# Kernel optimization log

Measured on AMD Instinct MI355X. Metric: run time of the kernel, lower is better.

Reference implementation:

```python
import jax, jax.numpy as jnp
import numpy as np

# dims: batch B, seq T, d_model C, expert_hidden H, n_experts E (top-1 routing)
B, T, C, H, E = 1, 256, 1024, 2048, 8
STD = 0.02


def setup_inputs() -> dict:
    key = jax.random.key(0)
    ks = jax.random.split(key, 8)
    f32 = jnp.float32
    return {
        "x": jax.random.normal(ks[0], (B, T, C), f32),
        "up": jax.random.normal(ks[1], (E, H, C), f32) * STD,
        "gate": jax.random.normal(ks[2], (E, H, C), f32) * STD,
        "down": jax.random.normal(ks[3], (E, C, H), f32) * STD,
        "router": jax.random.normal(ks[4], (E, C), f32) * STD,
        "w_up_s": jax.random.normal(ks[5], (H, C), f32) * STD,
        "w_gate_s": jax.random.normal(ks[6], (H, C), f32) * STD,
        "w_down_s": jax.random.normal(ks[7], (C, H), f32) * STD,
    }


def reference(x, up, gate, down, router, w_up_s, w_gate_s, w_down_s):
    b, t, c = x.shape
    x_ = x.reshape(b * t, c)                      # [BT, C]
    # top-1 router (gates are implicitly 1.0)
    logits = x_ @ router.T                        # [BT, E]
    idx = jnp.argmax(logits, axis=-1)             # [BT]
    onehot = jax.nn.one_hot(idx, router.shape[0], dtype=x.dtype)  # [BT, E]
    # dense all-expert SwiGLU, combined with one-hot (same math as per-token gather)
    u = jnp.einsum('bc,ehc->ebh', x_, up)         # [E, BT, H]
    g = jnp.einsum('bc,ehc->ebh', x_, gate)       # [E, BT, H]
    h = jax.nn.silu(g) * u                        # [E, BT, H]
    ye = jnp.einsum('ebh,ech->ebc', h, down)      # [E, BT, C]
    y = jnp.einsum('ebc,be->bc', ye, onehot)      # [BT, C]
    # shared expert residual
    ys = (jax.nn.silu(x_ @ w_gate_s.T) * (x_ @ w_up_s.T)) @ w_down_s.T
    return (y + ys).reshape(b, t, c)
```

## Files before the change

### kernel.cpp

```cpp
#include <hip/hip_runtime.h>
#include <hip/hip_bf16.h>

#define T_TOK 256
#define C_DIM 1024
#define H_DIM 2048
#define E_NUM 8

typedef __attribute__((ext_vector_type(4))) float f32x4;
typedef __attribute__((ext_vector_type(8))) short short8;

#define WS_CNT    0
#define WS_LIST   1024
#define WS_XBF    16384
#define WS_HBUF   (1u<<20)
#define WS_HSBUF  (2u<<20)
#define WS_YS     (3u<<20)

__device__ __forceinline__ ushort f2bf(float f) {
    __hip_bfloat16 h = __float2bfloat16(f);
    return *reinterpret_cast<ushort*>(&h);
}

__device__ __forceinline__ ushort4 f2bf4(float4 v) {
    ushort4 r; r.x = f2bf(v.x); r.y = f2bf(v.y); r.z = f2bf(v.z); r.w = f2bf(v.w);
    return r;
}

__device__ __forceinline__ ushort4 f2bf4v(f32x4 v) {
    ushort4 r; r.x = f2bf(v[0]); r.y = f2bf(v[1]); r.z = f2bf(v[2]); r.w = f2bf(v[3]);
    return r;
}

__device__ __forceinline__ void gload16(const void* g, void* l) {
    __builtin_amdgcn_global_load_lds((const __attribute__((address_space(1))) void*)g,
                                     (__attribute__((address_space(3))) void*)l, 16, 0, 0);
}

#define MFMA(a, b, c) __builtin_amdgcn_mfma_f32_16x16x32_bf16((a), (b), (c), 0, 0, 0)

#define VMWAIT(N) do { asm volatile("s_waitcnt vmcnt(" #N ")" ::: "memory"); \
                       __builtin_amdgcn_sched_barrier(0); } while (0)
#define LGKWAIT() do { asm volatile("s_waitcnt lgkmcnt(0)" ::: "memory"); \
                       __builtin_amdgcn_sched_barrier(0); } while (0)
#define BAR() do { __builtin_amdgcn_s_barrier(); \
                   __builtin_amdgcn_sched_barrier(0); } while (0)

__global__ __launch_bounds__(256) void router_kernel(
    const float* __restrict__ x, const float* __restrict__ router,
    int* __restrict__ cnt, int* __restrict__ list, ushort* __restrict__ xbf)
{
    const int t = blockIdx.x;
    const int tid = threadIdx.x;
    float4 xv = reinterpret_cast<const float4*>(x + (size_t)t * C_DIM)[tid];
    *reinterpret_cast<ushort4*>(xbf + (size_t)t * C_DIM + tid * 4) = f2bf4(xv);

    float p[E_NUM];
#pragma unroll
    for (int e = 0; e < E_NUM; e++) {
        float4 rv = reinterpret_cast<const float4*>(router + (size_t)e * C_DIM)[tid];
        p[e] = xv.x * rv.x + xv.y * rv.y + xv.z * rv.z + xv.w * rv.w;
    }
#pragma unroll
    for (int e = 0; e < E_NUM; e++) {
#pragma unroll
        for (int off = 32; off >= 1; off >>= 1)
            p[e] += __shfl_down(p[e], off, 64);
    }
    __shared__ float red[E_NUM][4];
    const int lane = tid & 63, wv = tid >> 6;
    if (lane == 0) {
#pragma unroll
        for (int e = 0; e < E_NUM; e++) red[e][wv] = p[e];
    }
    __syncthreads();
    if (tid == 0) {
        float best = -3.4e38f; int bi = 0;
#pragma unroll
        for (int e = 0; e < E_NUM; e++) {
            float v = red[e][0] + red[e][1] + red[e][2] + red[e][3];
            if (v > best) { best = v; bi = e; }
        }
        int pos = atomicAdd(&cnt[bi], 1);
        list[bi * T_TOK + pos] = t;
    }
}

__global__ __launch_bounds__(256, 3) void ug_mfma(
    const ushort* __restrict__ xbf, const float* __restrict__ up, const float* __restrict__ gate,
    const float* __restrict__ w_up_s, const float* __restrict__ w_gate_s,
    const int* __restrict__ cnt, const int* __restrict__ list,
    ushort* __restrict__ hbuf, ushort* __restrict__ hsbuf)
{
    const int e = blockIdx.x, by = blockIdx.y, tt = blockIdx.z;
    const bool sh = (e == E_NUM);
    const int n = sh ? T_TOK : cnt[e];
    if (tt * 32 >= n) return;
    const int tid = threadIdx.x, lane = tid & 63, wv = tid >> 6;
    const int lc = lane & 15, kg = lane >> 4;

    __shared__ __align__(16) char smem[32768];
    ushort* Xl  = (ushort*)smem;
    ushort* WuL = (ushort*)(smem + 16384);
    ushort* WgL = (ushort*)(smem + 24576);
    __shared__ int toks_s[32];

    if (tid < 32) {
        int t = tt * 32 + tid;
        toks_s[tid] = (t < n) ? (sh ? t : list[e * T_TOK + t]) : -1;
    }
    __syncthreads();

    const int h0 = by * 16;
    const float* __restrict__ ubase = (sh ? w_up_s   : up   + (size_t)e * H_DIM * C_DIM) + (size_t)h0 * C_DIM;
    const float* __restrict__ gbase = (sh ? w_gate_s : gate + (size_t)e * H_DIM * C_DIM) + (size_t)h0 * C_DIM;

    f32x4 wreg[8];
#define W_LOAD(tc) do { _Pragma("unroll") for (int i = 0; i < 8; i++) { \
        int row_ = wv * 4 + (i & 3); \
        const float* b_ = (i < 4) ? ubase : gbase; \
        const f32x4* p_ = reinterpret_cast<const f32x4*>(b_ + (size_t)row_ * C_DIM + (tc) * 256 + lane * 4); \
        wreg[i] = (sh || i < 4) ? *p_ : __builtin_nontemporal_load(p_); \
    } } while (0)

#define W_WRITE() do { _Pragma("unroll") for (int i = 0; i < 8; i++) { \
        int row_ = wv * 4 + (i & 3); \
        ushort* WL_ = (i < 4) ? WuL : WgL; \
        int pos_ = ((lane >> 1) & ~7) | (((lane >> 1) ^ row_) & 7); \
        *reinterpret_cast<ushort4*>(WL_ + row_ * 256 + pos_ * 8 + (lane & 1) * 4) = f2bf4v(wreg[i]); \
    } } while (0)

#define X_STAGE(tc) do { _Pragma("unroll") for (int i = 0; i < 4; i++) { \
        int j_ = wv * 4 + i; \
        int row_ = 2 * j_ + (lane >> 5); \
        int p_ = lane & 31; \
        int su_ = (p_ & ~7) | ((p_ ^ row_) & 7); \
        int tok_ = toks_s[row_]; if (tok_ < 0) tok_ = 0; \
        gload16(xbf + (size_t)tok_ * C_DIM + (tc) * 256 + su_ * 8, (void*)(Xl + j_ * 512)); \
    } } while (0)

    f32x4 au0 = {0,0,0,0}, au1 = {0,0,0,0}, ag0 = {0,0,0,0}, ag1 = {0,0,0,0};
#define COMPUTE() do { _Pragma("unroll") for (int k32 = 0; k32 < 2; k32++) { \
        int ku_ = wv * 8 + k32 * 4 + kg; \
        int up_ = (ku_ & ~7) | ((ku_ ^ lc) & 7); \
        short8 a0_ = *reinterpret_cast<const short8*>(Xl + lc * 256 + up_ * 8); \
        short8 a1_ = *reinterpret_cast<const short8*>(Xl + (16 + lc) * 256 + up_ * 8); \
        short8 bu_ = *reinterpret_cast<const short8*>(WuL + lc * 256 + up_ * 8); \
        short8 bg_ = *reinterpret_cast<const short8*>(WgL + lc * 256 + up_ * 8); \
        au0 = MFMA(a0_, bu_, au0); au1 = MFMA(a1_, bu_, au1); \
        ag0 = MFMA(a0_, bg_, ag0); ag1 = MFMA(a1_, bg_, ag1); \
    } } while (0)

    W_LOAD(0);
#pragma unroll
    for (int t = 0; t < 4; t++) {
        X_STAGE(t);
        W_WRITE();
        if (t < 3) W_LOAD(t + 1);
        __syncthreads();
        COMPUTE();
        __syncthreads();
    }
#undef W_LOAD
#undef W_WRITE
#undef X_STAGE
#undef COMPUTE

    f32x4* red = (f32x4*)smem;
    red[(wv * 4 + 0) * 64 + lane] = au0;
    red[(wv * 4 + 1) * 64 + lane] = au1;
    red[(wv * 4 + 2) * 64 + lane] = ag0;
    red[(wv * 4 + 3) * 64 + lane] = ag1;
    __syncthreads();
    if (tid < 128) {
        const int m = tid >> 6, ln = tid & 63, lc_ = ln & 15, kg_ = ln >> 4;
        f32x4 su = red[(0 + m) * 64 + ln];
        su += red[(4 + m) * 64 + ln];
        su += red[(8 + m) * 64 + ln];
        su += red[(12 + m) * 64 + ln];
        f32x4 sg = red[(2 + m) * 64 + ln];
        sg += red[(6 + m) * 64 + ln];
        sg += red[(10 + m) * 64 + ln];
        sg += red[(14 + m) * 64 + ln];
        ushort* __restrict__ outp = sh ? hsbuf : hbuf;
#pragma unroll
        for (int j = 0; j < 4; j++) {
            int tok = toks_s[m * 16 + kg_ * 4 + j];
            if (tok >= 0) {
                float g = sg[j], u = su[j];
                outp[(size_t)tok * H_DIM + h0 + lc_] = f2bf(u * (g / (1.f + __expf(-g))));
            }
        }
    }
}

__global__ __launch_bounds__(256, 2) void down_mfma(
    const float* __restrict__ dwn, const float* __restrict__ w_down_s,
    const ushort* __restrict__ hbuf, const ushort* __restrict__ hsbuf,
    const int* __restrict__ cnt, const int* __restrict__ list,
    float* __restrict__ y, float* __restrict__ yspart)
{
    const int e = blockIdx.x, by = blockIdx.y, tt = blockIdx.z;
    const bool sh = (e == E_NUM);
    const int n = sh ? T_TOK : cnt[e];
    if (tt * 32 >= n) return;
    const int tid = threadIdx.x, lane = tid & 63, wv = tid >> 6;
    const int lc = lane & 15, kg = lane >> 4;

    __shared__ __align__(16) char smem[49152];
    ushort* Hl  = (ushort*)smem;
    ushort* WdL = (ushort*)(smem + 32768);
    __shared__ int toks_s[32];

    if (tid < 32) {
        int t = tt * 32 + tid;
        toks_s[tid] = (t < n) ? (sh ? t : list[e * T_TOK + t]) : -1;
    }
    __syncthreads();

    const int c0 = by * 16;
    const float* __restrict__ dbase = (sh ? w_down_s : dwn + (size_t)e * C_DIM * H_DIM) + (size_t)c0 * H_DIM;
    const ushort* __restrict__ hin = sh ? hsbuf : hbuf;

    float4 wreg[4];
#define W_LOAD(tc) do { _Pragma("unroll") for (int i = 0; i < 4; i++) { \
        int row_ = wv * 4 + i; \
        wreg[i] = *reinterpret_cast<const float4*>(dbase + (size_t)row_ * H_DIM + (tc) * 256 + lane * 4); \
    } } while (0)

#define W_WRITE(bf) do { _Pragma("unroll") for (int i = 0; i < 4; i++) { \
        int row_ = wv * 4 + i; \
        int pos_ = ((lane >> 1) & ~7) | (((lane >> 1) ^ row_) & 7); \
        *reinterpret_cast<ushort4*>(WdL + (bf) * 4096 + row_ * 256 + pos_ * 8 + (lane & 1) * 4) = f2bf4(wreg[i]); \
    } } while (0)

#define H_STAGE(tc, bf) do { _Pragma("unroll") for (int i = 0; i < 4; i++) { \
        int j_ = wv * 4 + i; \
        int row_ = 2 * j_ + (lane >> 5); \
        int p_ = lane & 31; \
        int su_ = (p_ & ~7) | ((p_ ^ row_) & 7); \
        int tok_ = toks_s[row_]; if (tok_ < 0) tok_ = 0; \
        gload16(hin + (size_t)tok_ * H_DIM + (tc) * 256 + su_ * 8, (void*)(Hl + (bf) * 8192 + j_ * 512)); \
    } } while (0)

    f32x4 ac0 = {0,0,0,0}, ac1 = {0,0,0,0};
#define COMPUTE(bf) do { _Pragma("unroll") for (int k32 = 0; k32 < 2; k32++) { \
        int ku_ = wv * 8 + k32 * 4 + kg; \
        int up_ = (ku_ & ~7) | ((ku_ ^ lc) & 7); \
        short8 a0_ = *reinterpret_cast<const short8*>(Hl + (bf) * 8192 + lc * 256 + up_ * 8); \
        short8 a1_ = *reinterpret_cast<const short8*>(Hl + (bf) * 8192 + (16 + lc) * 256 + up_ * 8); \
        short8 bd_ = *reinterpret_cast<const short8*>(WdL + (bf) * 4096 + lc * 256 + up_ * 8); \
        ac0 = MFMA(a0_, bd_, ac0); ac1 = MFMA(a1_, bd_, ac1); \
    } } while (0)

    W_LOAD(0);
    H_STAGE(0, 0);
    VMWAIT(4);
    W_WRITE(0);
    W_LOAD(1);
    H_STAGE(1, 1);
    LGKWAIT();
    VMWAIT(8);
    BAR();

#pragma unroll
    for (int t = 0; t < 8; t++) {
        COMPUTE(t & 1);
        if (t < 7) {
            VMWAIT(4);
            W_WRITE((t + 1) & 1);
            if (t < 6) W_LOAD(t + 2);
            LGKWAIT();
        }
        BAR();
        if (t < 6) H_STAGE(t + 2, t & 1);
        if (t < 6)      { VMWAIT(8); }
        else if (t == 6){ VMWAIT(0); }
        BAR();
    }

    f32x4* red = (f32x4*)smem;
    red[(wv * 2 + 0) * 64 + lane] = ac0;
    red[(wv * 2 + 1) * 64 + lane] = ac1;
    __syncthreads();
    if (tid < 128) {
        const int m = tid >> 6, ln = tid & 63, lc_ = ln & 15, kg_ = ln >> 4;
        f32x4 s = red[(0 + m) * 64 + ln];
        s += red[(2 + m) * 64 + ln];
        s += red[(4 + m) * 64 + ln];
        s += red[(6 + m) * 64 + ln];
        float* __restrict__ outp = sh ? yspart : y;
#pragma unroll
        for (int j = 0; j < 4; j++) {
            int tok = toks_s[m * 16 + kg_ * 4 + j];
            if (tok >= 0) outp[(size_t)tok * C_DIM + c0 + lc_] = s[j];
        }
    }
#undef W_LOAD
#undef W_WRITE
#undef H_STAGE
#undef COMPUTE
}

__global__ __launch_bounds__(256) void add_kernel(float* __restrict__ y, const float* __restrict__ ys)
{
    int i = blockIdx.x * 256 + threadIdx.x;
    float4 a = reinterpret_cast<float4*>(y)[i];
    float4 b = reinterpret_cast<const float4*>(ys)[i];
    a.x += b.x; a.y += b.y; a.z += b.z; a.w += b.w;
    reinterpret_cast<float4*>(y)[i] = a;
}

extern "C" void kernel_launch(void* const* d_in, const int* in_sizes, int n_in,
                              void* d_out, int out_size, void* d_ws, size_t ws_size,
                              hipStream_t stream)
{
    const float* x        = (const float*)d_in[0];
    const float* up       = (const float*)d_in[1];
    const float* gate     = (const float*)d_in[2];
    const float* dwn      = (const float*)d_in[3];
    const float* router   = (const float*)d_in[4];
    const float* w_up_s   = (const float*)d_in[5];
    const float* w_gate_s = (const float*)d_in[6];
    const float* w_down_s = (const float*)d_in[7];

    char* ws = (char*)d_ws;
    int* cnt      = (int*)(ws + WS_CNT);
    int* list     = (int*)(ws + WS_LIST);
    ushort* xbf   = (ushort*)(ws + WS_XBF);
    ushort* hbuf  = (ushort*)(ws + WS_HBUF);
    ushort* hsbuf = (ushort*)(ws + WS_HSBUF);
    float* yspart = (float*)(ws + WS_YS);
    float* y = (float*)d_out;

    hipMemsetAsync(cnt, 0, E_NUM * sizeof(int), stream);
    router_kernel<<<T_TOK, 256, 0, stream>>>(x, router, cnt, list, xbf);
    ug_mfma<<<dim3(E_NUM + 1, H_DIM / 16, 8), 256, 0, stream>>>(
        xbf, up, gate, w_up_s, w_gate_s, cnt, list, hbuf, hsbuf);
    down_mfma<<<dim3(E_NUM + 1, C_DIM / 16, 8), 256, 0, stream>>>(
        dwn, w_down_s, hbuf, hsbuf, cnt, list, y, yspart);
    add_kernel<<<(T_TOK * C_DIM / 4) / 256, 256, 0, stream>>>(y, yspart);
}
```

Measured before the change: 86.82 us.

## Pre-convert up/gate weights to bf16 in a separate pass before MFMA

New measurement: 100.5 us. +15.7%, slower.

```diff
diff --git a/kernel.cpp b/kernel.cpp
--- a/kernel.cpp
+++ b/kernel.cpp
@@ -9,12 +9,20 @@
 typedef __attribute__((ext_vector_type(4))) float f32x4;
 typedef __attribute__((ext_vector_type(8))) short short8;
 
-#define WS_CNT    0
-#define WS_LIST   1024
-#define WS_XBF    16384
-#define WS_HBUF   (1u<<20)
-#define WS_HSBUF  (2u<<20)
-#define WS_YS     (3u<<20)
+#define WS_CNT     0
+#define WS_LIST    1024
+#define WS_XBF     16384
+#define WS_HBUF    (1u<<20)
+#define WS_HSBUF   (2u<<20)
+#define WS_YS      (3u<<20)
+#define WS_UPBF    (8u<<20)
+#define WS_GATEBF  (44u<<20)
+#define WS_UPSBF   (80u<<20)
+#define WS_GATESBF (85u<<20)
+#define WS_NEED    (90ull<<20)
+
+#define N_EW  16777216ull
+#define N_SW  2097152ull
 
 __device__ __forceinline__ ushort f2bf(float f) {
     __hip_bfloat16 h = __float2bfloat16(f);
@@ -29,6 +37,15 @@
 __device__ __forceinline__ ushort4 f2bf4v(f32x4 v) {
     ushort4 r; r.x = f2bf(v[0]); r.y = f2bf(v[1]); r.z = f2bf(v[2]); r.w = f2bf(v[3]);
     return r;
+}
+
+__device__ __forceinline__ short8 pack8(float4 a, float4 b) {
+    short8 s;
+    s[0] = (short)f2bf(a.x); s[1] = (short)f2bf(a.y);
+    s[2] = (short)f2bf(a.z); s[3] = (short)f2bf(a.w);
+    s[4] = (short)f2bf(b.x); s[5] = (short)f2bf(b.y);
+    s[6] = (short)f2bf(b.z); s[7] = (short)f2bf(b.w);
+    return s;
 }
 
 __device__ __forceinline__ void gload16(const void* g, void* l) {
@@ -45,6 +62,24 @@
 #define BAR() do { __builtin_amdgcn_s_barrier(); \
                    __builtin_amdgcn_sched_barrier(0); } while (0)
 
+__global__ __launch_bounds__(256) void wprep(
+    const float* __restrict__ up, const float* __restrict__ gate,
+    const float* __restrict__ ups, const float* __restrict__ gates,
+    ushort* __restrict__ upbf, ushort* __restrict__ gatebf,
+    ushort* __restrict__ upsbf, ushort* __restrict__ gatesbf)
+{
+    size_t gid = (size_t)blockIdx.x * 256 + threadIdx.x;
+    size_t base = gid * 8;
+    const float* src; ushort* dst;
+    if (base < N_EW)               { src = up    + base;                dst = upbf    + base; }
+    else if (base < 2 * N_EW)      { src = gate  + (base - N_EW);       dst = gatebf  + (base - N_EW); }
+    else if (base < 2 * N_EW + N_SW){ src = ups  + (base - 2 * N_EW);   dst = upsbf   + (base - 2 * N_EW); }
+    else                           { src = gates + (base - 2 * N_EW - N_SW); dst = gatesbf + (base - 2 * N_EW - N_SW); }
+    float4 a = *reinterpret_cast<const float4*>(src);
+    float4 b = *reinterpret_cast<const float4*>(src + 4);
+    *reinterpret_cast<short8*>(dst) = pack8(a, b);
+}
+
 __global__ __launch_bounds__(256) void router_kernel(
     const float* __restrict__ x, const float* __restrict__ router,
     int* __restrict__ cnt, int* __restrict__ list, ushort* __restrict__ xbf)
@@ -85,9 +120,10 @@
     }
 }
 
-__global__ __launch_bounds__(256, 3) void ug_mfma(
-    const ushort* __restrict__ xbf, const float* __restrict__ up, const float* __restrict__ gate,
-    const float* __restrict__ w_up_s, const float* __restrict__ w_gate_s,
+__global__ __launch_bounds__(256, 3) void ug_mfma_bf(
+    const ushort* __restrict__ xbf, const ushort* __restrict__ upbf,
+    const ushort* __restrict__ gatebf, const ushort* __restrict__ upsbf,
+    const ushort* __restrict__ gatesbf,
     const int* __restrict__ cnt, const int* __restrict__ list,
     ushort* __restrict__ hbuf, ushort* __restrict__ hsbuf)
 {
@@ -111,6 +147,106 @@
     __syncthreads();
 
     const int h0 = by * 16;
+    const ushort* __restrict__ ubase = (sh ? upsbf   : upbf   + (size_t)e * H_DIM * C_DIM) + (size_t)h0 * C_DIM;
+    const ushort* __restrict__ gbase = (sh ? gatesbf : gatebf + (size_t)e * H_DIM * C_DIM) + (size_t)h0 * C_DIM;
+
+#define W_STAGE(tc) do { _Pragma("unroll") for (int i = 0; i < 4; i++) { \
+        int j_ = wv * 2 + (i & 1); \
+        const ushort* b_ = (i < 2) ? ubase : gbase; \
+        ushort* L_ = (i < 2) ? WuL : WgL; \
+        int row_ = 2 * j_ + (lane >> 5); \
+        int p_ = lane & 31; \
+        int su_ = (p_ & ~7) | ((p_ ^ row_) & 7); \
+        gload16(b_ + (size_t)row_ * C_DIM + (tc) * 256 + su_ * 8, (void*)(L_ + j_ * 512)); \
+    } } while (0)
+
+#define X_STAGE(tc) do { _Pragma("unroll") for (int i = 0; i < 4; i++) { \
+        int j_ = wv * 4 + i; \
+        int row_ = 2 * j_ + (lane >> 5); \
+        int p_ = lane & 31; \
+        int su_ = (p_ & ~7) | ((p_ ^ row_) & 7); \
+        int tok_ = toks_s[row_]; if (tok_ < 0) tok_ = 0; \
+        gload16(xbf + (size_t)tok_ * C_DIM + (tc) * 256 + su_ * 8, (void*)(Xl + j_ * 512)); \
+    } } while (0)
+
+    f32x4 au0 = {0,0,0,0}, au1 = {0,0,0,0}, ag0 = {0,0,0,0}, ag1 = {0,0,0,0};
+#define COMPUTE() do { _Pragma("unroll") for (int k32 = 0; k32 < 2; k32++) { \
+        int ku_ = wv * 8 + k32 * 4 + kg; \
+        int up_ = (ku_ & ~7) | ((ku_ ^ lc) & 7); \
+        short8 a0_ = *reinterpret_cast<const short8*>(Xl + lc * 256 + up_ * 8); \
+        short8 a1_ = *reinterpret_cast<const short8*>(Xl + (16 + lc) * 256 + up_ * 8); \
+        short8 bu_ = *reinterpret_cast<const short8*>(WuL + lc * 256 + up_ * 8); \
+        short8 bg_ = *reinterpret_cast<const short8*>(WgL + lc * 256 + up_ * 8); \
+        au0 = MFMA(a0_, bu_, au0); au1 = MFMA(a1_, bu_, au1); \
+        ag0 = MFMA(a0_, bg_, ag0); ag1 = MFMA(a1_, bg_, ag1); \
+    } } while (0)
+
+#pragma unroll
+    for (int t = 0; t < 4; t++) {
+        X_STAGE(t);
+        W_STAGE(t);
+        __syncthreads();
+        COMPUTE();
+        __syncthreads();
+    }
+#undef W_STAGE
+#undef X_STAGE
+#undef COMPUTE
+
+    f32x4* red = (f32x4*)smem;
+    red[(wv * 4 + 0) * 64 + lane] = au0;
+    red[(wv * 4 + 1) * 64 + lane] = au1;
+    red[(wv * 4 + 2) * 64 + lane] = ag0;
+    red[(wv * 4 + 3) * 64 + lane] = ag1;
+    __syncthreads();
+    if (tid < 128) {
+        const int m = tid >> 6, ln = tid & 63, lc_ = ln & 15, kg_ = ln >> 4;
+        f32x4 su = red[(0 + m) * 64 + ln];
+        su += red[(4 + m) * 64 + ln];
+        su += red[(8 + m) * 64 + ln];
+        su += red[(12 + m) * 64 + ln];
+        f32x4 sg = red[(2 + m) * 64 + ln];
+        sg += red[(6 + m) * 64 + ln];
+        sg += red[(10 + m) * 64 + ln];
+        sg += red[(14 + m) * 64 + ln];
+        ushort* __restrict__ outp = sh ? hsbuf : hbuf;
+#pragma unroll
+        for (int j = 0; j < 4; j++) {
+            int tok = toks_s[m * 16 + kg_ * 4 + j];
+            if (tok >= 0) {
+                float g = sg[j], u = su[j];
+                outp[(size_t)tok * H_DIM + h0 + lc_] = f2bf(u * (g / (1.f + __expf(-g))));
+            }
+        }
+    }
+}
+
+__global__ __launch_bounds__(256, 3) void ug_mfma_direct(
+    const ushort* __restrict__ xbf, const float* __restrict__ up, const float* __restrict__ gate,
+    const float* __restrict__ w_up_s, const float* __restrict__ w_gate_s,
+    const int* __restrict__ cnt, const int* __restrict__ list,
+    ushort* __restrict__ hbuf, ushort* __restrict__ hsbuf)
+{
+    const int e = blockIdx.x, by = blockIdx.y, tt = blockIdx.z;
+    const bool sh = (e == E_NUM);
+    const int n = sh ? T_TOK : cnt[e];
+    if (tt * 32 >= n) return;
+    const int tid = threadIdx.x, lane = tid & 63, wv = tid >> 6;
+    const int lc = lane & 15, kg = lane >> 4;
+
+    __shared__ __align__(16) char smem[32768];
+    ushort* Xl  = (ushort*)smem;
+    ushort* WuL = (ushort*)(smem + 16384);
+    ushort* WgL = (ushort*)(smem + 24576);
+    __shared__ int toks_s[32];
+
+    if (tid < 32) {
+        int t = tt * 32 + tid;
+        toks_s[tid] = (t < n) ? (sh ? t : list[e * T_TOK + t]) : -1;
+    }
+    __syncthreads();
+
+    const int h0 = by * 16;
     const float* __restrict__ ubase = (sh ? w_up_s   : up   + (size_t)e * H_DIM * C_DIM) + (size_t)h0 * C_DIM;
     const float* __restrict__ gbase = (sh ? w_gate_s : gate + (size_t)e * H_DIM * C_DIM) + (size_t)h0 * C_DIM;
 
@@ -118,8 +254,7 @@
 #define W_LOAD(tc) do { _Pragma("unroll") for (int i = 0; i < 8; i++) { \
         int row_ = wv * 4 + (i & 3); \
         const float* b_ = (i < 4) ? ubase : gbase; \
-        const f32x4* p_ = reinterpret_cast<const f32x4*>(b_ + (size_t)row_ * C_DIM + (tc) * 256 + lane * 4); \
-        wreg[i] = (sh || i < 4) ? *p_ : __builtin_nontemporal_load(p_); \
+        wreg[i] = *reinterpret_cast<const f32x4*>(b_ + (size_t)row_ * C_DIM + (tc) * 256 + lane * 4); \
     } } while (0)
 
 #define W_WRITE() do { _Pragma("unroll") for (int i = 0; i < 8; i++) { \
@@ -324,18 +459,31 @@
     const float* w_down_s = (const float*)d_in[7];
 
     char* ws = (char*)d_ws;
-    int* cnt      = (int*)(ws + WS_CNT);
-    int* list     = (int*)(ws + WS_LIST);
-    ushort* xbf   = (ushort*)(ws + WS_XBF);
-    ushort* hbuf  = (ushort*)(ws + WS_HBUF);
-    ushort* hsbuf = (ushort*)(ws + WS_HSBUF);
-    float* yspart = (float*)(ws + WS_YS);
+    int* cnt       = (int*)(ws + WS_CNT);
+    int* list      = (int*)(ws + WS_LIST);
+    ushort* xbf    = (ushort*)(ws + WS_XBF);
+    ushort* hbuf   = (ushort*)(ws + WS_HBUF);
+    ushort* hsbuf  = (ushort*)(ws + WS_HSBUF);
+    float* yspart  = (float*)(ws + WS_YS);
     float* y = (float*)d_out;
 
     hipMemsetAsync(cnt, 0, E_NUM * sizeof(int), stream);
     router_kernel<<<T_TOK, 256, 0, stream>>>(x, router, cnt, list, xbf);
-    ug_mfma<<<dim3(E_NUM + 1, H_DIM / 16, 8), 256, 0, stream>>>(
-        xbf, up, gate, w_up_s, w_gate_s, cnt, list, hbuf, hsbuf);
+
+    if (ws_size >= WS_NEED) {
+        ushort* upbf    = (ushort*)(ws + WS_UPBF);
+        ushort* gatebf  = (ushort*)(ws + WS_GATEBF);
+        ushort* upsbf   = (ushort*)(ws + WS_UPSBF);
+        ushort* gatesbf = (ushort*)(ws + WS_GATESBF);
+        wprep<<<18432, 256, 0, stream>>>(up, gate, w_up_s, w_gate_s,
+                                         upbf, gatebf, upsbf, gatesbf);
+        ug_mfma_bf<<<dim3(E_NUM + 1, H_DIM / 16, 8), 256, 0, stream>>>(
+            xbf, upbf, gatebf, upsbf, gatesbf, cnt, list, hbuf, hsbuf);
+    } else {
+        ug_mfma_direct<<<dim3(E_NUM + 1, H_DIM / 16, 8), 256, 0, stream>>>(
+            xbf, up, gate, w_up_s, w_gate_s, cnt, list, hbuf, hsbuf);
+    }
+
     down_mfma<<<dim3(E_NUM + 1, C_DIM / 16, 8), 256, 0, stream>>>(
         dwn, w_down_s, hbuf, hsbuf, cnt, list, y, yspart);
     add_kernel<<<(T_TOK * C_DIM / 4) / 256, 256, 0, stream>>>(y, yspart);
```
